# Optimization experiments

Measured on AMD Instinct MI355X. Metric: run time of the kernel, lower is better.

## Reference

```python
import jax, jax.numpy as jnp
import numpy as np

EPS = 1e-5  # BatchNorm eps (torch default)
K = 16      # num_neighbors


def _bn(x, gamma, beta, axes):
    # training-mode BatchNorm (biased variance), channel axis = 1
    mu = x.mean(axes, keepdims=True)
    var = x.var(axes, keepdims=True)
    shp = [1] * x.ndim
    shp[1] = -1
    return (x - mu) * jax.lax.rsqrt(var + EPS) * gamma.reshape(shp) + beta.reshape(shp)


def setup_inputs() -> dict:
    key = jax.random.key(0)
    ks = jax.random.split(key, 6)
    B, C, N, E = 4, 3, 4096, 256
    s = lambda k_, shp, fan: jax.random.normal(k_, shp, jnp.float32) * np.float32(1.0 / np.sqrt(fan))
    return {
        "x": jax.random.normal(ks[0], (B, C, N), jnp.float32),
        "g1": jnp.ones((C,), jnp.float32), "b1": jnp.zeros((C,), jnp.float32),
        "W1": s(ks[1], (E, C), C), "bw1": jnp.zeros((E,), jnp.float32),
        "g2a": jnp.ones((C,), jnp.float32), "b2a": jnp.zeros((C,), jnp.float32),
        "W2a": s(ks[2], (E, C), C),
        "g2b": jnp.ones((E,), jnp.float32), "b2b": jnp.zeros((E,), jnp.float32),
        "W2b": s(ks[3], (E, E), E),
        "Wf": s(ks[4], (E, 2 * E), 2 * E), "bf": jnp.zeros((E,), jnp.float32),
    }


def reference(x, g1, b1, W1, bw1, g2a, b2a, W2a, g2b, b2b, W2b, Wf, bf):
    B, C, N = x.shape
    xn = _bn(x, g1, b1, (0, 2))                               # BatchNorm1d
    point_emb = jnp.einsum('ec,bcn->ben', W1, xn) + bw1[None, :, None]  # conv1 (1x1)
    # dist = -||xi - xj||; torch topk(dist, largest=False) picks the K LARGEST
    # distances. Squared distance is monotone in the norm, so top_k on d2 gives
    # identical indices without materializing [B,3,N,N].
    x2 = jnp.sum(xn * xn, axis=1)                             # [B,N]
    d2 = x2[:, :, None] + x2[:, None, :] - 2.0 * jnp.einsum('bcn,bcm->bnm', xn, xn)
    _, idx = jax.lax.top_k(d2, min(K, N))                     # [B,N,K]
    idx = idx[:, :, 1:]                                       # original loop skips index 0
    gathered = jax.vmap(lambda xb, ib: xb[:, ib])(xn, idx)    # [B,C,N,K-1]
    neigh = gathered - xn[:, :, :, None]                      # edge features
    h = _bn(neigh, g2a, b2a, (0, 2, 3))                       # BatchNorm2d(Cin)
    h = jnp.einsum('ec,bcnk->benk', W2a, h)                   # 1x1 conv, no bias
    h = jax.nn.gelu(_bn(h, g2b, b2b, (0, 2, 3)), approximate=False)
    h = jnp.einsum('fe,benk->bfnk', W2b, h)                   # 1x1 conv, no bias
    neigh_emb = h.max(-1)                                     # max over neighbors
    feat = jnp.concatenate([point_emb, neigh_emb], axis=1)    # [B,2E,N]
    return jnp.einsum('of,bfn->bon', Wf, feat) + bf[None, :, None]
```

## Files before the change

kernel.cpp:

```cpp
#include <hip/hip_runtime.h>
#include <float.h>
#include <math.h>

#define EPS 1e-5f
constexpr int B = 4, C = 3, N = 4096, E = 256;
constexpr int KNN = 15;
constexpr int BN_ = B * N;
constexpr int P = 8;
constexpr int SR  = 264;
constexpr int SRF = 520;

typedef short bf8 __attribute__((ext_vector_type(8)));
typedef float f4  __attribute__((ext_vector_type(4)));

static __device__ __forceinline__ unsigned short f2bf(float f) {
    union { float f; unsigned int u; } v; v.f = f;
    unsigned int r = v.u + 0x7FFFu + ((v.u >> 16) & 1u);
    return (unsigned short)(r >> 16);
}
static __device__ __forceinline__ bf8 ld_bf8(const unsigned short* p) {
    return *(const bf8*)p;
}
static __device__ __forceinline__ float gelu_t(float v) {
    float z = v * fmaf(v * v, 0.07135482f, 1.59576912f);
    float r = __builtin_amdgcn_rcpf(1.f + __expf(z));
    return fmaf(-v, r, v);
}

__global__ void bn1_stats(const float* __restrict__ x, float* __restrict__ bn1) {
    int c = blockIdx.x, t = threadIdx.x;
    float s = 0.f, ss = 0.f;
    for (int i4 = t; i4 < BN_ / 4; i4 += 256) {
        int b = i4 >> 10, n4 = i4 & 1023;
        float4 v = ((const float4*)(x + (b * C + c) * N))[n4];
        s += v.x + v.y + v.z + v.w;
        ss += v.x * v.x + v.y * v.y + v.z * v.z + v.w * v.w;
    }
    __shared__ float rs_[256], rss_[256];
    rs_[t] = s; rss_[t] = ss; __syncthreads();
    for (int w = 128; w > 0; w >>= 1) {
        if (t < w) { rs_[t] += rs_[t + w]; rss_[t] += rss_[t + w]; }
        __syncthreads();
    }
    if (t == 0) {
        float mu = rs_[0] / (float)BN_;
        float var = rss_[0] / (float)BN_ - mu * mu;
        bn1[c] = mu; bn1[3 + c] = rsqrtf(var + EPS);
    }
}

__global__ void compute_xn_cvt(const float* __restrict__ x,
                               const float* __restrict__ g1,
                               const float* __restrict__ b1,
                               const float* __restrict__ bn1,
                               float4* __restrict__ xn4,
                               const float* __restrict__ W2b, const float* __restrict__ Wf,
                               unsigned short* __restrict__ w2b_t, unsigned short* __restrict__ wf_t) {
    int blk = blockIdx.x;
    if (blk < BN_ / 256) {
        int i = blk * 256 + threadIdx.x;
        int b = i >> 12, n = i & (N - 1);
        float v[3];
        #pragma unroll
        for (int c = 0; c < C; c++)
            v[c] = (x[(b * C + c) * N + n] - bn1[c]) * bn1[3 + c] * g1[c] + b1[c];
        float4 o; o.x = v[0]; o.y = v[1]; o.z = v[2];
        o.w = v[0] * v[0] + v[1] * v[1] + v[2] * v[2];
        xn4[i] = o;
        return;
    }
    int ch = (blk - BN_ / 256) * 256 + threadIdx.x;
    if (ch < 8192) {
        int lane = ch & 63, kb = (ch >> 6) & 7, ft16 = ch >> 9;
        int row = ft16 * 16 + (lane & 15);
        int col = kb * 32 + (lane >> 4) * 8;
        #pragma unroll
        for (int j = 0; j < 8; j++)
            w2b_t[ch * 8 + j] = f2bf(W2b[row * 256 + col + j]);
    } else {
        int c2 = ch - 8192;
        int lane = c2 & 63, kb = (c2 >> 6) & 15, ot = c2 >> 10;
        int row = ot * 16 + (lane & 15);
        int col = kb * 32 + (lane >> 4) * 8;
        #pragma unroll
        for (int j = 0; j < 8; j++)
            wf_t[c2 * 8 + j] = f2bf(Wf[row * 512 + col + j]);
    }
}

__global__ void __launch_bounds__(256, 4) knn_kernel(const float4* __restrict__ xn4,
                                                     unsigned short* __restrict__ idxout,
                                                     float* __restrict__ S9) {
    __shared__ float smom[4][15][9];
    int w = threadIdx.x >> 6, lane = threadIdx.x & 63;
    int i = blockIdx.x * 4 + w;
    int b = i >> 12, n = i & (N - 1);
    const float4* xb = xn4 + b * N;
    float4 qv = xb[n];
    float d[64];
    #pragma unroll
    for (int s = 0; s < 64; s++) {
        float4 p = xb[s * 64 + lane];
        d[s] = qv.w + p.w - 2.f * (qv.x * p.x + qv.y * p.y + qv.z * p.z);
    }
    float cm[8];
    #pragma unroll
    for (int c = 0; c < 8; c++) {
        float v = d[c * 8];
        #pragma unroll
        for (int s = 1; s < 8; s++) v = fmaxf(v, d[c * 8 + s]);
        cm[c] = v;
    }
    float bv = cm[0];
    #pragma unroll
    for (int c = 1; c < 8; c++) bv = fmaxf(bv, cm[c]);

    int myj = 0;
    for (int r = 0; r < 16; r++) {
        float wv = bv;
        #pragma unroll
        for (int off = 32; off > 0; off >>= 1)
            wv = fmaxf(wv, __shfl_xor(wv, off));
        unsigned long long msk = __ballot(bv == wv);
        int wl = __ffsll(msk) - 1;
        int gi = 0;
        if (lane == wl) {
            int cstar = 0; bool got = false;
            #pragma unroll
            for (int c = 0; c < 8; c++) {
                bool h = !got && (cm[c] == bv);
                cstar = h ? c : cstar;
                got = got || h;
            }
            int slot = 0;
            #pragma unroll
            for (int c = 0; c < 8; c++) {
                if (c == cstar) {
                    bool g2 = false;
                    #pragma unroll
                    for (int s = 0; s < 8; s++) {
                        bool h = !g2 && (d[c * 8 + s] == bv);
                        slot = h ? (c * 8 + s) : slot;
                        g2 = g2 || h;
                    }
                    #pragma unroll
                    for (int s = 0; s < 8; s++)
                        d[c * 8 + s] = (c * 8 + s == slot) ? -FLT_MAX : d[c * 8 + s];
                    float v = d[c * 8];
                    #pragma unroll
                    for (int s = 1; s < 8; s++) v = fmaxf(v, d[c * 8 + s]);
                    cm[c] = v;
                }
            }
            bv = cm[0];
            #pragma unroll
            for (int c = 1; c < 8; c++) bv = fmaxf(bv, cm[c]);
            gi = slot * 64 + lane;
        }
        int g = __shfl(gi, wl);
        if (lane == r - 1) myj = g;
    }

    bool act = lane < 15;
    if (act) idxout[i * KNN + lane] = (unsigned short)myj;
    float4 pj = xb[act ? myj : n];
    float v0 = pj.x - qv.x, v1 = pj.y - qv.y, v2 = pj.z - qv.z;
    if (act) {
        float* mm = smom[w][lane];
        mm[0] = v0; mm[1] = v1; mm[2] = v2;
        mm[3] = v0 * v0; mm[4] = v1 * v1; mm[5] = v2 * v2;
        mm[6] = v0 * v1; mm[7] = v0 * v2; mm[8] = v1 * v2;
    }
    __syncthreads();
    int t = threadIdx.x;
    if (t < 36) {
        int wsel = t / 9, j = t % 9;
        float a = 0.f;
        #pragma unroll
        for (int u = 0; u < 15; u++) a += smom[wsel][u][j];
        atomicAdd(&S9[((blockIdx.x * 4 + wsel) & 63) * 9 + j], a);
    }
}

__global__ void finalize_stats(const float* __restrict__ S9,
                               const float* __restrict__ g2a, const float* __restrict__ b2a,
                               const float* __restrict__ W2a,
                               const float* __restrict__ g2b, const float* __restrict__ b2b,
                               float* __restrict__ ab, float4* __restrict__ wsb) {
    const float cnt = (float)(BN_ * KNN);
    __shared__ float S[9];
    __shared__ float alpha[3], beta[3], mu[3], Ehh[3][3];
    int t = threadIdx.x;
    if (t < 9) {
        float a = 0.f;
        for (int u = 0; u < 64; u++) a += S9[u * 9 + t];
        S[t] = a;
    }
    __syncthreads();
    if (t == 0) {
        float m[3];
        float s2[3][3];
        s2[0][0] = S[3]; s2[1][1] = S[4]; s2[2][2] = S[5];
        s2[0][1] = s2[1][0] = S[6]; s2[0][2] = s2[2][0] = S[7]; s2[1][2] = s2[2][1] = S[8];
        for (int c = 0; c < 3; c++) {
            m[c] = S[c] / cnt;
            float var = s2[c][c] / cnt - m[c] * m[c];
            alpha[c] = g2a[c] * rsqrtf(var + EPS);
            beta[c]  = b2a[c] - m[c] * alpha[c];
            mu[c] = m[c];
            ab[c] = alpha[c]; ab[3 + c] = beta[c];
        }
        for (int c = 0; c < 3; c++)
            for (int cc = 0; cc < 3; cc++)
                Ehh[c][cc] = alpha[c] * alpha[cc] * (s2[c][cc] / cnt)
                           + alpha[c] * beta[cc] * m[c]
                           + beta[c] * alpha[cc] * m[cc]
                           + beta[c] * beta[cc];
    }
    __syncthreads();
    int e = t;
    float wv[3], Eh[3];
    for (int c = 0; c < 3; c++) { wv[c] = W2a[e * 3 + c]; Eh[c] = alpha[c] * mu[c] + beta[c]; }
    float mean = wv[0] * Eh[0] + wv[1] * Eh[1] + wv[2] * Eh[2];
    float m2 = 0.f;
    for (int c = 0; c < 3; c++)
        for (int cc = 0; cc < 3; cc++) m2 += wv[c] * wv[cc] * Ehh[c][cc];
    float var = m2 - mean * mean;
    float s = g2b[e] * rsqrtf(var + EPS);
    float4 o;
    o.x = wv[0] * s; o.y = wv[1] * s; o.z = wv[2] * s; o.w = b2b[e] - mean * s;
    wsb[e] = o;
}

__global__ void __launch_bounds__(512, 4) fused_final(
        const float4* __restrict__ xn4, const unsigned short* __restrict__ idx,
        const float* __restrict__ ab,
        const float4* __restrict__ wsb,
        const unsigned short* __restrict__ w2b_t,
        const float* __restrict__ W1, const float* __restrict__ bw1,
        const unsigned short* __restrict__ wf_t, const float* __restrict__ bfv,
        float* __restrict__ out) {
    __shared__ __align__(16) unsigned short hh_bf[128 * SR];
    __shared__ __align__(16) unsigned short feat_bf[8 * SRF];
    __shared__ __align__(16) float4 hhat4[P][16];
    int i0 = blockIdx.x * P;
    int t = threadIdx.x;
    int b = i0 >> 12, n0 = i0 & (N - 1);
    const float4* xb = xn4 + b * N;

    if (t < P * KNN) {
        int p = t / KNN, k = t % KNN;
        int j = idx[(i0 + p) * KNN + k];
        float4 pj = xb[j];
        float4 pn = xb[n0 + p];
        float4 h;
        h.x = ab[0] * (pj.x - pn.x) + ab[3];
        h.y = ab[1] * (pj.y - pn.y) + ab[4];
        h.z = ab[2] * (pj.z - pn.z) + ab[5];
        h.w = 0.f;
        hhat4[p][k] = h;
    }
    __syncthreads();

    {
        int e = t & 255;
        int ph = t >> 8;
        float4 w4 = wsb[e];
        #pragma unroll
        for (int pp = 0; pp < 4; pp++) {
            int p = ph * 4 + pp;
            float g0 = 0.f;
            #pragma unroll
            for (int k = 0; k < KNN; k++) {
                float4 hv = hhat4[p][k];
                float v = fmaf(w4.x, hv.x, fmaf(w4.y, hv.y, fmaf(w4.z, hv.z, w4.w)));
                float g = gelu_t(v);
                hh_bf[(16 * p + k) * SR + e] = f2bf(g);
                if (k == 0) g0 = g;
            }
            hh_bf[(16 * p + 15) * SR + e] = f2bf(g0);
            float4 pv = xb[n0 + p];
            feat_bf[p * SRF + e] = f2bf(bw1[e] + W1[e * 3] * pv.x
                       + W1[e * 3 + 1] * pv.y + W1[e * 3 + 2] * pv.z);
        }
    }
    __syncthreads();

    int w = t >> 6, lane = t & 63;
    int m = lane & 15, q = lane >> 4;

    {
        #pragma unroll
        for (int f = 0; f < 2; f++) {
            int ft = w * 2 + f;
            bf8 a[8];
            #pragma unroll
            for (int kb = 0; kb < 8; kb++)
                a[kb] = ld_bf8(w2b_t + ft * 4096 + kb * 512 + lane * 8);
            #pragma unroll 1
            for (int pr = 0; pr < 4; pr++) {
                bf8 hfr[2][8];
                #pragma unroll
                for (int pi = 0; pi < 2; pi++)
                    #pragma unroll
                    for (int kb = 0; kb < 8; kb++)
                        hfr[pi][kb] = ld_bf8(&hh_bf[(16 * (pr * 2 + pi) + m) * SR + kb * 32 + q * 8]);
                #pragma unroll
                for (int pi = 0; pi < 2; pi++) {
                    f4 acc = {0.f, 0.f, 0.f, 0.f};
                    #pragma unroll
                    for (int kb = 0; kb < 8; kb++)
                        acc = __builtin_amdgcn_mfma_f32_16x16x32_bf16(hfr[pi][kb], a[kb], acc, 0, 0, 0);
                    float mx = fmaxf(fmaxf(acc[0], acc[1]), fmaxf(acc[2], acc[3]));
                    mx = fmaxf(mx, __shfl_xor(mx, 16));
                    mx = fmaxf(mx, __shfl_xor(mx, 32));
                    if (lane < 16)
                        feat_bf[(pr * 2 + pi) * SRF + E + ft * 16 + lane] = f2bf(mx);
                }
            }
        }
    }
    __syncthreads();

    {
        bf8 fb[16];
        #pragma unroll
        for (int kb = 0; kb < 16; kb++)
            fb[kb] = ld_bf8(&feat_bf[(m & 7) * SRF + kb * 32 + q * 8]);
        #pragma unroll
        for (int o2 = 0; o2 < 2; o2++) {
            int ot = w * 2 + o2;
            f4 acc = {0.f, 0.f, 0.f, 0.f};
            #pragma unroll
            for (int kb = 0; kb < 16; kb++) {
                bf8 a = ld_bf8(wf_t + ot * 8192 + kb * 512 + lane * 8);
                acc = __builtin_amdgcn_mfma_f32_16x16x32_bf16(a, fb[kb], acc, 0, 0, 0);
            }
            if (m < P) {
                int o0 = ot * 16 + 4 * q;
                out[(b * E + o0 + 0) * N + n0 + m] = acc[0] + bfv[o0 + 0];
                out[(b * E + o0 + 1) * N + n0 + m] = acc[1] + bfv[o0 + 1];
                out[(b * E + o0 + 2) * N + n0 + m] = acc[2] + bfv[o0 + 2];
                out[(b * E + o0 + 3) * N + n0 + m] = acc[3] + bfv[o0 + 3];
            }
        }
    }
}

extern "C" void kernel_launch(void* const* d_in, const int* in_sizes, int n_in,
                              void* d_out, int out_size, void* d_ws, size_t ws_size,
                              hipStream_t stream) {
    (void)in_sizes; (void)n_in; (void)out_size; (void)ws_size;
    const float* x   = (const float*)d_in[0];
    const float* g1  = (const float*)d_in[1];
    const float* b1  = (const float*)d_in[2];
    const float* W1  = (const float*)d_in[3];
    const float* bw1 = (const float*)d_in[4];
    const float* g2a = (const float*)d_in[5];
    const float* b2a = (const float*)d_in[6];
    const float* W2a = (const float*)d_in[7];
    const float* g2b = (const float*)d_in[8];
    const float* b2b = (const float*)d_in[9];
    const float* W2b = (const float*)d_in[10];
    const float* Wf  = (const float*)d_in[11];
    const float* bfv = (const float*)d_in[12];
    float* out = (float*)d_out;

    char* ws = (char*)d_ws;
    size_t off = 0;
    auto alloc = [&](size_t bytes) { size_t o = off; off = (off + bytes + 255) & ~(size_t)255; return o; };
    float4* xn4           = (float4*)(ws + alloc(sizeof(float4) * BN_));
    unsigned short* idx   = (unsigned short*)(ws + alloc(sizeof(unsigned short) * BN_ * KNN));
    float* bn1            = (float*)(ws + alloc(sizeof(float) * 8));
    float* S9             = (float*)(ws + alloc(sizeof(float) * 64 * 9));
    float* ab             = (float*)(ws + alloc(sizeof(float) * 8));
    float4* wsb           = (float4*)(ws + alloc(sizeof(float4) * E));
    unsigned short* w2bt  = (unsigned short*)(ws + alloc(sizeof(unsigned short) * E * E));
    unsigned short* wft   = (unsigned short*)(ws + alloc(sizeof(unsigned short) * E * 2 * E));

    hipMemsetAsync(S9, 0, sizeof(float) * 64 * 9, stream);

    bn1_stats<<<C, 256, 0, stream>>>(x, bn1);
    compute_xn_cvt<<<BN_ / 256 + (8192 + 16384) / 256, 256, 0, stream>>>(
        x, g1, b1, bn1, xn4, W2b, Wf, w2bt, wft);
    knn_kernel<<<BN_ / 4, 256, 0, stream>>>(xn4, idx, S9);
    finalize_stats<<<1, 256, 0, stream>>>(S9, g2a, b2a, W2a, g2b, b2b, ab, wsb);
    fused_final<<<BN_ / P, 512, 0, stream>>>(xn4, idx, ab, wsb, w2bt, W1, bw1, wft, bfv, out);
}
```

Measured before the change: 247.8 us.

## Fold BN1 stats, memset, and finalize_stats into neighboring kernels to cut launches

Removes the separate bn1_stats kernel by having each of the 64 normalization blocks redundantly reduce all three channels' statistics over the full input. The S9 memset moves into the conversion kernel, and the finalize_stats kernel is dropped. Every fused_final block now recomputes the BN2a/BN2b parameters from S9 itself. This cuts three launches and serial dependencies, paid for with redundant reductions: 64 blocks each read all of x, and every one of the 2048 fused_final blocks adds a reduction prologue and an extra barrier.

```diff
diff --git a/kernel.cpp b/kernel.cpp
--- a/kernel.cpp
+++ b/kernel.cpp
@@ -27,49 +27,59 @@
     return fmaf(-v, r, v);
 }
 
-__global__ void bn1_stats(const float* __restrict__ x, float* __restrict__ bn1) {
-    int c = blockIdx.x, t = threadIdx.x;
-    float s = 0.f, ss = 0.f;
-    for (int i4 = t; i4 < BN_ / 4; i4 += 256) {
-        int b = i4 >> 10, n4 = i4 & 1023;
-        float4 v = ((const float4*)(x + (b * C + c) * N))[n4];
-        s += v.x + v.y + v.z + v.w;
-        ss += v.x * v.x + v.y * v.y + v.z * v.z + v.w * v.w;
-    }
-    __shared__ float rs_[256], rss_[256];
-    rs_[t] = s; rss_[t] = ss; __syncthreads();
-    for (int w = 128; w > 0; w >>= 1) {
-        if (t < w) { rs_[t] += rs_[t + w]; rss_[t] += rss_[t + w]; }
+__global__ void __launch_bounds__(256) compute_xn_cvt(
+        const float* __restrict__ x,
+        const float* __restrict__ g1, const float* __restrict__ b1,
+        float4* __restrict__ xn4,
+        const float* __restrict__ W2b, const float* __restrict__ Wf,
+        unsigned short* __restrict__ w2b_t, unsigned short* __restrict__ wf_t,
+        float* __restrict__ S9) {
+    int blk = blockIdx.x;
+    int t = threadIdx.x;
+    if (blk < 64) {
+        __shared__ float red[256][6];
+        float s[3] = {0.f, 0.f, 0.f}, ss[3] = {0.f, 0.f, 0.f};
+        #pragma unroll
+        for (int c = 0; c < 3; c++) {
+            for (int i4 = t; i4 < BN_ / 4; i4 += 256) {
+                int b = i4 >> 10, n4 = i4 & 1023;
+                float4 v = ((const float4*)(x + (b * C + c) * N))[n4];
+                s[c]  += v.x + v.y + v.z + v.w;
+                ss[c] += v.x * v.x + v.y * v.y + v.z * v.z + v.w * v.w;
+            }
+        }
+        #pragma unroll
+        for (int c = 0; c < 3; c++) { red[t][c] = s[c]; red[t][3 + c] = ss[c]; }
         __syncthreads();
-    }
-    if (t == 0) {
-        float mu = rs_[0] / (float)BN_;
-        float var = rss_[0] / (float)BN_ - mu * mu;
-        bn1[c] = mu; bn1[3 + c] = rsqrtf(var + EPS);
-    }
-}
-
-__global__ void compute_xn_cvt(const float* __restrict__ x,
-                               const float* __restrict__ g1,
-                               const float* __restrict__ b1,
-                               const float* __restrict__ bn1,
-                               float4* __restrict__ xn4,
-                               const float* __restrict__ W2b, const float* __restrict__ Wf,
-                               unsigned short* __restrict__ w2b_t, unsigned short* __restrict__ wf_t) {
-    int blk = blockIdx.x;
-    if (blk < BN_ / 256) {
-        int i = blk * 256 + threadIdx.x;
+        for (int w = 128; w > 0; w >>= 1) {
+            if (t < w) {
+                #pragma unroll
+                for (int j = 0; j < 6; j++) red[t][j] += red[t + w][j];
+            }
+            __syncthreads();
+        }
+        float mu[3], rs[3];
+        #pragma unroll
+        for (int c = 0; c < 3; c++) {
+            mu[c] = red[0][c] / (float)BN_;
+            float var = red[0][3 + c] / (float)BN_ - mu[c] * mu[c];
+            rs[c] = rsqrtf(var + EPS);
+        }
+        int i = blk * 256 + t;
         int b = i >> 12, n = i & (N - 1);
         float v[3];
         #pragma unroll
         for (int c = 0; c < C; c++)
-            v[c] = (x[(b * C + c) * N + n] - bn1[c]) * bn1[3 + c] * g1[c] + b1[c];
+            v[c] = (x[(b * C + c) * N + n] - mu[c]) * rs[c] * g1[c] + b1[c];
         float4 o; o.x = v[0]; o.y = v[1]; o.z = v[2];
         o.w = v[0] * v[0] + v[1] * v[1] + v[2] * v[2];
         xn4[i] = o;
         return;
     }
-    int ch = (blk - BN_ / 256) * 256 + threadIdx.x;
+    if (blk == 64) {
+        for (int j = t; j < 64 * 9; j += 256) S9[j] = 0.f;
+    }
+    int ch = (blk - 64) * 256 + t;
     if (ch < 8192) {
         int lane = ch & 63, kb = (ch >> 6) & 7, ft16 = ch >> 9;
         int row = ft16 * 16 + (lane & 15);
@@ -182,60 +192,12 @@
     }
 }
 
-__global__ void finalize_stats(const float* __restrict__ S9,
-                               const float* __restrict__ g2a, const float* __restrict__ b2a,
-                               const float* __restrict__ W2a,
-                               const float* __restrict__ g2b, const float* __restrict__ b2b,
-                               float* __restrict__ ab, float4* __restrict__ wsb) {
-    const float cnt = (float)(BN_ * KNN);
-    __shared__ float S[9];
-    __shared__ float alpha[3], beta[3], mu[3], Ehh[3][3];
-    int t = threadIdx.x;
-    if (t < 9) {
-        float a = 0.f;
-        for (int u = 0; u < 64; u++) a += S9[u * 9 + t];
-        S[t] = a;
-    }
-    __syncthreads();
-    if (t == 0) {
-        float m[3];
-        float s2[3][3];
-        s2[0][0] = S[3]; s2[1][1] = S[4]; s2[2][2] = S[5];
-        s2[0][1] = s2[1][0] = S[6]; s2[0][2] = s2[2][0] = S[7]; s2[1][2] = s2[2][1] = S[8];
-        for (int c = 0; c < 3; c++) {
-            m[c] = S[c] / cnt;
-            float var = s2[c][c] / cnt - m[c] * m[c];
-            alpha[c] = g2a[c] * rsqrtf(var + EPS);
-            beta[c]  = b2a[c] - m[c] * alpha[c];
-            mu[c] = m[c];
-            ab[c] = alpha[c]; ab[3 + c] = beta[c];
-        }
-        for (int c = 0; c < 3; c++)
-            for (int cc = 0; cc < 3; cc++)
-                Ehh[c][cc] = alpha[c] * alpha[cc] * (s2[c][cc] / cnt)
-                           + alpha[c] * beta[cc] * m[c]
-                           + beta[c] * alpha[cc] * m[cc]
-                           + beta[c] * beta[cc];
-    }
-    __syncthreads();
-    int e = t;
-    float wv[3], Eh[3];
-    for (int c = 0; c < 3; c++) { wv[c] = W2a[e * 3 + c]; Eh[c] = alpha[c] * mu[c] + beta[c]; }
-    float mean = wv[0] * Eh[0] + wv[1] * Eh[1] + wv[2] * Eh[2];
-    float m2 = 0.f;
-    for (int c = 0; c < 3; c++)
-        for (int cc = 0; cc < 3; cc++) m2 += wv[c] * wv[cc] * Ehh[c][cc];
-    float var = m2 - mean * mean;
-    float s = g2b[e] * rsqrtf(var + EPS);
-    float4 o;
-    o.x = wv[0] * s; o.y = wv[1] * s; o.z = wv[2] * s; o.w = b2b[e] - mean * s;
-    wsb[e] = o;
-}
-
 __global__ void __launch_bounds__(512, 4) fused_final(
         const float4* __restrict__ xn4, const unsigned short* __restrict__ idx,
-        const float* __restrict__ ab,
-        const float4* __restrict__ wsb,
+        const float* __restrict__ S9,
+        const float* __restrict__ g2a, const float* __restrict__ b2a,
+        const float* __restrict__ W2a,
+        const float* __restrict__ g2b, const float* __restrict__ b2b,
         const unsigned short* __restrict__ w2b_t,
         const float* __restrict__ W1, const float* __restrict__ bw1,
         const unsigned short* __restrict__ wf_t, const float* __restrict__ bfv,
@@ -243,10 +205,59 @@
     __shared__ __align__(16) unsigned short hh_bf[128 * SR];
     __shared__ __align__(16) unsigned short feat_bf[8 * SRF];
     __shared__ __align__(16) float4 hhat4[P][16];
+    __shared__ float falpha[3], fbeta[3], fmu[3], fEhh[3][3];
     int i0 = blockIdx.x * P;
     int t = threadIdx.x;
     int b = i0 >> 12, n0 = i0 & (N - 1);
     const float4* xb = xn4 + b * N;
+    const float cnt = (float)(BN_ * KNN);
+
+    if (t < 64) {
+        float v[9];
+        #pragma unroll
+        for (int j = 0; j < 9; j++) v[j] = S9[t * 9 + j];
+        #pragma unroll
+        for (int off = 32; off > 0; off >>= 1)
+            #pragma unroll
+            for (int j = 0; j < 9; j++) v[j] += __shfl_xor(v[j], off);
+        if (t == 0) {
+            float s2[3][3];
+            s2[0][0] = v[3]; s2[1][1] = v[4]; s2[2][2] = v[5];
+            s2[0][1] = s2[1][0] = v[6]; s2[0][2] = s2[2][0] = v[7]; s2[1][2] = s2[2][1] = v[8];
+            float al[3], be[3], m[3];
+            #pragma unroll
+            for (int c = 0; c < 3; c++) {
+                m[c] = v[c] / cnt;
+                float var = s2[c][c] / cnt - m[c] * m[c];
+                al[c] = g2a[c] * rsqrtf(var + EPS);
+                be[c] = b2a[c] - m[c] * al[c];
+                falpha[c] = al[c]; fbeta[c] = be[c]; fmu[c] = m[c];
+            }
+            #pragma unroll
+            for (int c = 0; c < 3; c++)
+                #pragma unroll
+                for (int cc = 0; cc < 3; cc++)
+                    fEhh[c][cc] = al[c] * al[cc] * (s2[c][cc] / cnt)
+                                + al[c] * be[cc] * m[c] + be[c] * al[cc] * m[cc] + be[c] * be[cc];
+        }
+    }
+    __syncthreads();
+
+    float4 w4;
+    {
+        int e = t & 255;
+        float wv0 = W2a[e * 3], wv1 = W2a[e * 3 + 1], wv2 = W2a[e * 3 + 2];
+        float Eh0 = falpha[0] * fmu[0] + fbeta[0];
+        float Eh1 = falpha[1] * fmu[1] + fbeta[1];
+        float Eh2 = falpha[2] * fmu[2] + fbeta[2];
+        float mean = wv0 * Eh0 + wv1 * Eh1 + wv2 * Eh2;
+        float m2 = wv0 * (wv0 * fEhh[0][0] + wv1 * fEhh[0][1] + wv2 * fEhh[0][2])
+                 + wv1 * (wv0 * fEhh[1][0] + wv1 * fEhh[1][1] + wv2 * fEhh[1][2])
+                 + wv2 * (wv0 * fEhh[2][0] + wv1 * fEhh[2][1] + wv2 * fEhh[2][2]);
+        float var = m2 - mean * mean;
+        float s = g2b[e] * rsqrtf(var + EPS);
+        w4.x = wv0 * s; w4.y = wv1 * s; w4.z = wv2 * s; w4.w = b2b[e] - mean * s;
+    }
 
     if (t < P * KNN) {
         int p = t / KNN, k = t % KNN;
@@ -254,9 +265,9 @@
         float4 pj = xb[j];
         float4 pn = xb[n0 + p];
         float4 h;
-        h.x = ab[0] * (pj.x - pn.x) + ab[3];
-        h.y = ab[1] * (pj.y - pn.y) + ab[4];
-        h.z = ab[2] * (pj.z - pn.z) + ab[5];
+        h.x = falpha[0] * (pj.x - pn.x) + fbeta[0];
+        h.y = falpha[1] * (pj.y - pn.y) + fbeta[1];
+        h.z = falpha[2] * (pj.z - pn.z) + fbeta[2];
         h.w = 0.f;
         hhat4[p][k] = h;
     }
@@ -265,7 +276,6 @@
     {
         int e = t & 255;
         int ph = t >> 8;
-        float4 w4 = wsb[e];
         #pragma unroll
         for (int pp = 0; pp < 4; pp++) {
             int p = ph * 4 + pp;
@@ -371,19 +381,12 @@
     auto alloc = [&](size_t bytes) { size_t o = off; off = (off + bytes + 255) & ~(size_t)255; return o; };
     float4* xn4           = (float4*)(ws + alloc(sizeof(float4) * BN_));
     unsigned short* idx   = (unsigned short*)(ws + alloc(sizeof(unsigned short) * BN_ * KNN));
-    float* bn1            = (float*)(ws + alloc(sizeof(float) * 8));
     float* S9             = (float*)(ws + alloc(sizeof(float) * 64 * 9));
-    float* ab             = (float*)(ws + alloc(sizeof(float) * 8));
-    float4* wsb           = (float4*)(ws + alloc(sizeof(float4) * E));
     unsigned short* w2bt  = (unsigned short*)(ws + alloc(sizeof(unsigned short) * E * E));
     unsigned short* wft   = (unsigned short*)(ws + alloc(sizeof(unsigned short) * E * 2 * E));
 
-    hipMemsetAsync(S9, 0, sizeof(float) * 64 * 9, stream);
-
-    bn1_stats<<<C, 256, 0, stream>>>(x, bn1);
-    compute_xn_cvt<<<BN_ / 256 + (8192 + 16384) / 256, 256, 0, stream>>>(
-        x, g1, b1, bn1, xn4, W2b, Wf, w2bt, wft);
+    compute_xn_cvt<<<160, 256, 0, stream>>>(x, g1, b1, xn4, W2b, Wf, w2bt, wft, S9);
     knn_kernel<<<BN_ / 4, 256, 0, stream>>>(xn4, idx, S9);
-    finalize_stats<<<1, 256, 0, stream>>>(S9, g2a, b2a, W2a, g2b, b2b, ab, wsb);
-    fused_final<<<BN_ / P, 512, 0, stream>>>(xn4, idx, ab, wsb, w2bt, W1, bw1, wft, bfv, out);
-}
+    fused_final<<<BN_ / P, 512, 0, stream>>>(xn4, idx, S9, g2a, b2a, W2a, g2b, b2b,
+                                             w2bt, W1, bw1, wft, bfv, out);
+}
```

New measurement: 254.8 us. +2.9%, slower.
